# Kernel optimization log

Hardware: AMD Instinct MI355X
Metric: run time of the kernel (lower is better)

The kernel has to match this reference:

```python
import jax, jax.numpy as jnp
import numpy as np

N, T, H, NENV, L = 8192, 48, 256, 10, 2
NIN = 1 + 2 + NENV + 1 + 2  # x, coords(2), env(NENV), areas, bird_uv(2) = 16


def setup_inputs() -> dict:
    key = jax.random.key(0)
    ks = jax.random.split(key, 10)
    x = jax.random.normal(ks[0], (N, T), dtype=jnp.float32)
    coords = jax.random.normal(ks[1], (N, 2), dtype=jnp.float32)
    env = jax.random.normal(ks[2], (N, NENV, T), dtype=jnp.float32)
    areas = jax.random.uniform(ks[3], (N,), dtype=jnp.float32)
    bird_uv = jax.random.normal(ks[4], (N, 2, T), dtype=jnp.float32)
    # input2hidden: Linear(NIN, H, bias=False), kaiming-normal (fan_in = NIN)
    W_in = jax.random.normal(ks[5], (H, NIN), dtype=jnp.float32) * np.sqrt(2.0 / NIN)
    # LSTMCell params per layer: weight_ih [4H,H], weight_hh [4H,H], biases [4H]
    k_lstm = 1.0 / np.sqrt(H)
    W_ih = jax.random.uniform(ks[6], (L, 4 * H, H), minval=-k_lstm, maxval=k_lstm, dtype=jnp.float32)
    W_hh = jax.random.uniform(ks[7], (L, 4 * H, H), minval=-k_lstm, maxval=k_lstm, dtype=jnp.float32)
    b_ih = jax.random.uniform(ks[8], (L, 4 * H), minval=-k_lstm, maxval=k_lstm, dtype=jnp.float32)
    b_hh = jax.random.uniform(ks[9], (L, 4 * H), minval=-k_lstm, maxval=k_lstm, dtype=jnp.float32)
    return {"x": x, "coords": coords, "env": env, "areas": areas, "bird_uv": bird_uv,
            "W_in": W_in, "W_ih": W_ih, "W_hh": W_hh, "b_ih": b_ih, "b_hh": b_hh}


def _lstm_cell(inp, h, c, w_ih, w_hh, bi, bh):
    # torch.nn.LSTMCell gate order: i, f, g, o
    gates = inp @ w_ih.T + bi + h @ w_hh.T + bh  # [N, 4H]
    i, f, g, o = jnp.split(gates, 4, axis=-1)
    i = jax.nn.sigmoid(i)
    f = jax.nn.sigmoid(f)
    g = jnp.tanh(g)
    o = jax.nn.sigmoid(o)
    c_new = f * c + i * g
    h_new = o * jnp.tanh(c_new)
    return h_new, c_new


def reference(x, coords, env, areas, bird_uv, W_in, W_ih, W_hh, b_ih, b_hh):
    # Build [N, NIN, T] feature tensor matching torch.cat([x, coords, env, areas, bird_uv], dim=1)
    feats = jnp.concatenate([
        x[:, None, :],                                            # [N,1,T]
        jnp.broadcast_to(coords[:, :, None], (N, 2, T)),          # [N,2,T]
        env,                                                      # [N,NENV,T]
        jnp.broadcast_to(areas[:, None, None], (N, 1, T)),        # [N,1,T]
        bird_uv,                                                  # [N,2,T]
    ], axis=1)
    # input2hidden applied to all timesteps at once: [T, N, H]
    proj = jnp.einsum('hf,nft->tnh', W_in, feats)

    def step(carry, inp_t):
        h, c = carry  # each [L, N, H]
        inp = inp_t
        hs, cs = [], []
        for l in range(L):  # dropout_p = 0 -> no dropout between layers
            hl, cl = _lstm_cell(inp, h[l], c[l], W_ih[l], W_hh[l], b_ih[l], b_hh[l])
            hs.append(hl)
            cs.append(cl)
            inp = hl
        return (jnp.stack(hs), jnp.stack(cs)), None

    h0 = jnp.zeros((L, N, H), dtype=x.dtype)
    c0 = jnp.zeros((L, N, H), dtype=x.dtype)
    (h, c), _ = jax.lax.scan(step, (h0, c0), proj)
    return h, c
```

## Files before the change

kernel.cpp:

```cpp
#include <hip/hip_runtime.h>
#include <hip/hip_bf16.h>
#include <cstdint>

#define NB 8192
#define TSTEPS 48

typedef __hip_bfloat16 bf16;
typedef short bf16x8 __attribute__((ext_vector_type(8)));
typedef float f32x4 __attribute__((ext_vector_type(4)));

__device__ __forceinline__ float sigf(float x) { return 1.0f / (1.0f + __expf(-x)); }
__device__ __forceinline__ float tanhf_fast(float x) { return 2.0f / (1.0f + __expf(-2.0f * x)) - 1.0f; }

__device__ __forceinline__ void gld_lds16(const void* g, void* l) {
  typedef const __attribute__((address_space(1))) unsigned int* gp_t;
  typedef __attribute__((address_space(3))) unsigned int* lp_t;
  __builtin_amdgcn_global_load_lds(reinterpret_cast<gp_t>(reinterpret_cast<uintptr_t>(g)),
                                   reinterpret_cast<lp_t>(reinterpret_cast<uintptr_t>(l)),
                                   16, 0, 0);
}

__global__ void feats_kernel(const float* __restrict__ x, const float* __restrict__ coords,
                             const float* __restrict__ env, const float* __restrict__ areas,
                             const float* __restrict__ bird, bf16* __restrict__ feats) {
  int idx = blockIdx.x * 256 + threadIdx.x;
  int n = idx & (NB - 1);
  int t = idx >> 13;
  __align__(16) bf16 v[32];
  v[0] = __float2bfloat16(x[n * TSTEPS + t]);
  v[1] = __float2bfloat16(coords[n * 2 + 0]);
  v[2] = __float2bfloat16(coords[n * 2 + 1]);
#pragma unroll
  for (int e = 0; e < 10; ++e) v[3 + e] = __float2bfloat16(env[(n * 10 + e) * TSTEPS + t]);
  v[13] = __float2bfloat16(areas[n]);
  v[14] = __float2bfloat16(bird[(n * 2 + 0) * TSTEPS + t]);
  v[15] = __float2bfloat16(bird[(n * 2 + 1) * TSTEPS + t]);
#pragma unroll
  for (int f = 16; f < 32; ++f) v[f] = __float2bfloat16(0.0f);
  bf16* dst = feats + (size_t)idx * 32;
#pragma unroll
  for (int c = 0; c < 4; ++c) ((bf16x8*)dst)[c] = ((const bf16x8*)v)[c];
}

__device__ __forceinline__ int orig_row(int jp) {
  int q = jp >> 7, g = (jp >> 5) & 3, s = jp & 31;
  return g * 256 + q * 32 + s;
}

__global__ void packA_kernel(const float* __restrict__ W_hh0, const float* __restrict__ W_ih0,
                             const float* __restrict__ W_in, bf16* __restrict__ WA) {
  int idx = blockIdx.x * 256 + threadIdx.x;
  int jp = idx / 288, col = idx % 288;
  int j = orig_row(jp);
  float val = 0.0f;
  if (col < 256) {
    val = W_hh0[j * 256 + col];
  } else if (col < 272) {
    int f = col - 256;
    float s = 0.0f;
    for (int k = 0; k < 256; ++k) s += W_ih0[j * 256 + k] * W_in[k * 16 + f];
    val = s;
  }
  WA[(size_t)jp * 288 + col] = __float2bfloat16(val);
}

__global__ void packB_kernel(const float* __restrict__ W_ih1, const float* __restrict__ W_hh1,
                             bf16* __restrict__ WB) {
  int idx = blockIdx.x * 256 + threadIdx.x;
  int jp = idx >> 9, col = idx & 511;
  int j = orig_row(jp);
  float val = (col < 256) ? W_ih1[j * 256 + col] : W_hh1[j * 256 + (col - 256)];
  WB[(size_t)jp * 512 + col] = __float2bfloat16(val);
}

__global__ void packBias_kernel(const float* __restrict__ b_ih, const float* __restrict__ b_hh,
                                float* __restrict__ bA, float* __restrict__ bB) {
  int idx = blockIdx.x * 256 + threadIdx.x;
  int layer = idx >> 10, jp = idx & 1023;
  int j = orig_row(jp);
  float v = b_ih[layer * 1024 + j] + b_hh[layer * 1024 + j];
  if (layer == 0) bA[jp] = v; else bB[jp] = v;
}

__global__ __launch_bounds__(256, 4) void lstm_step(
    const bf16* __restrict__ h0r, bf16* __restrict__ h0w,
    const bf16* __restrict__ h1r, bf16* __restrict__ h1w,
    const bf16* __restrict__ feats,
    const bf16* __restrict__ WA, const bf16* __restrict__ WB,
    const float* __restrict__ bA, const float* __restrict__ bB,
    float* __restrict__ c0, float* __restrict__ c1,
    float* __restrict__ out, int tA, int tB, int phase0, int lastA, int lastB) {
  __shared__ float Gs[64 * 132];
  bf16* As = (bf16*)Gs;
  bf16* Bs = As + 128 * 32;

  const int tid = threadIdx.x;
  const int wid = tid >> 6, lane = tid & 63;
  const int quad = lane >> 4, l16 = lane & 15;
  const int mb = (wid >> 1) * 64, nb = (wid & 1) * 64;
  const int rowbase = blockIdx.x * 128;
  const int q = blockIdx.y;
  const int isA = blockIdx.z + phase0;

  const bf16* Wp = isA ? WA : WB;
  const int KW = isA ? 288 : 512;
  const int KITERS = isA ? 9 : 16;
  const int t = isA ? tA : tB;

  f32x4 acc[4][4];
#pragma unroll
  for (int i = 0; i < 4; ++i)
#pragma unroll
    for (int j = 0; j < 4; ++j) acc[i][j] = f32x4{0.f, 0.f, 0.f, 0.f};

  const int arow = wid * 32 + (lane >> 2);
  const int achunk = (lane & 3) * 8;
  const bf16* WGrow = Wp + (size_t)(q * 128 + arow) * KW + achunk;
  bf16* lA = As + wid * 1024;
  bf16* lB = Bs + wid * 1024;

  for (int kb = 0; kb < KITERS; ++kb) {
    const bf16* Arow;
    int astr;
    if (isA && kb == 8) {
      Arow = feats + ((size_t)t * NB + rowbase) * 32;
      astr = 32;
    } else {
      const bf16* src = (!isA && kb >= 8) ? (h1r + (kb - 8) * 32) : (h0r + kb * 32);
      Arow = src + (size_t)rowbase * 256;
      astr = 256;
    }
    const bf16* ga = Arow + (size_t)arow * astr + achunk;
    const bf16* gb = WGrow + kb * 32;
    gld_lds16(ga, lA);
    gld_lds16(ga + (size_t)16 * astr, lA + 512);
    gld_lds16(gb, lB);
    gld_lds16(gb + (size_t)16 * KW, lB + 512);
    __syncthreads();
    bf16x8 af[4], bfr[4];
#pragma unroll
    for (int i = 0; i < 4; ++i) af[i] = *(const bf16x8*)&As[(mb + i * 16 + l16) * 32 + quad * 8];
#pragma unroll
    for (int j = 0; j < 4; ++j) bfr[j] = *(const bf16x8*)&Bs[(nb + j * 16 + l16) * 32 + quad * 8];
#pragma unroll
    for (int i = 0; i < 4; ++i)
#pragma unroll
      for (int j = 0; j < 4; ++j)
        acc[i][j] = __builtin_amdgcn_mfma_f32_16x16x32_bf16(af[i], bfr[j], acc[i][j], 0, 0, 0);
    __syncthreads();
  }

  const float* bias = isA ? bA : bB;
  float* cst = isA ? c0 : c1;
  bf16* hout = isA ? h0w : h1w;
  const int last = isA ? lastA : lastB;
  float* out_h = out + (size_t)(isA ? 0 : 1) * NB * 256;
  float* out_c = out + (size_t)(isA ? 2 : 3) * NB * 256;

  const int s = tid & 31;
  const int rg = tid >> 5;
  const float bi = bias[q * 128 + 0 + s];
  const float bf_ = bias[q * 128 + 32 + s];
  const float bg = bias[q * 128 + 64 + s];
  const float bo = bias[q * 128 + 96 + s];
  const int u = q * 32 + s;

  for (int half = 0; half < 2; ++half) {
    if ((wid >> 1) == half) {
#pragma unroll
      for (int i = 0; i < 4; ++i)
#pragma unroll
        for (int j = 0; j < 4; ++j)
#pragma unroll
          for (int r = 0; r < 4; ++r)
            Gs[(i * 16 + quad * 4 + r) * 132 + nb + j * 16 + l16] = acc[i][j][r];
    }
    __syncthreads();
#pragma unroll
    for (int it = 0; it < 8; ++it) {
      int rl = rg * 8 + it;
      int n = rowbase + half * 64 + rl;
      float gi = sigf(Gs[rl * 132 + 0 + s] + bi);
      float gf = sigf(Gs[rl * 132 + 32 + s] + bf_);
      float gg = tanhf_fast(Gs[rl * 132 + 64 + s] + bg);
      float go = sigf(Gs[rl * 132 + 96 + s] + bo);
      size_t ci = (size_t)n * 256 + u;
      float c = cst[ci];
      float cn = gf * c + gi * gg;
      float hn = go * tanhf_fast(cn);
      cst[ci] = cn;
      hout[ci] = __float2bfloat16(hn);
      if (last) {
        out_h[ci] = hn;
        out_c[ci] = cn;
      }
    }
    __syncthreads();
  }
}

extern "C" void kernel_launch(void* const* d_in, const int* in_sizes, int n_in,
                              void* d_out, int out_size, void* d_ws, size_t ws_size,
                              hipStream_t stream) {
  const float* x = (const float*)d_in[0];
  const float* coords = (const float*)d_in[1];
  const float* env = (const float*)d_in[2];
  const float* areas = (const float*)d_in[3];
  const float* bird = (const float*)d_in[4];
  const float* W_in = (const float*)d_in[5];
  const float* W_ih = (const float*)d_in[6];
  const float* W_hh = (const float*)d_in[7];
  const float* b_ih = (const float*)d_in[8];
  const float* b_hh = (const float*)d_in[9];
  float* out = (float*)d_out;

  const size_t MB = 1 << 20;
  char* w0 = (char*)d_ws;
  auto H0 = [&](int i) { return (bf16*)(w0 + (size_t)i * 8 * MB); };
  auto H1 = [&](int i) { return (bf16*)(w0 + 4 * MB + (size_t)i * 8 * MB); };
  float* c0 = (float*)(w0 + 16 * MB);
  float* c1 = (float*)(w0 + 24 * MB);
  bf16* feats = (bf16*)(w0 + 32 * MB);
  bf16* WA = (bf16*)(w0 + 56 * MB);
  bf16* WB = (bf16*)(w0 + 57 * MB);
  float* bA = (float*)(w0 + 58 * MB);
  float* bB = (float*)(w0 + 58 * MB + 4096);

  hipMemsetAsync(w0 + 8 * MB, 0, 24 * MB, stream);

  feats_kernel<<<(NB * TSTEPS) / 256, 256, 0, stream>>>(x, coords, env, areas, bird, feats);
  packA_kernel<<<(1024 * 288) / 256, 256, 0, stream>>>(W_hh, W_ih, W_in, WA);
  packB_kernel<<<(1024 * 512) / 256, 256, 0, stream>>>(W_ih + 1024 * 256, W_hh + 1024 * 256, WB);
  packBias_kernel<<<2048 / 256, 256, 0, stream>>>(b_ih, b_hh, bA, bB);

  lstm_step<<<dim3(64, 8, 1), 256, 0, stream>>>(
      H0(1), H0(0), H1(0), H1(1), feats, WA, WB, bA, bB, c0, c1, out,
      0, 0, 1, 0, 0);
  for (int s2 = 0; s2 <= 46; ++s2) {
    int pa = (s2 + 1) & 1, pb = s2 & 1;
    lstm_step<<<dim3(64, 8, 2), 256, 0, stream>>>(
        H0(pb), H0(pa), H1(pa), H1(pb), feats, WA, WB, bA, bB, c0, c1, out,
        s2 + 1, s2, 0, (s2 == 46), 0);
  }
  lstm_step<<<dim3(64, 8, 1), 256, 0, stream>>>(
      H0(1), H0(0), H1(0), H1(1), feats, WA, WB, bA, bB, c0, c1, out,
      0, 47, 0, 0, 1);
}
```

Baseline: 1.492 ms.

## Replace per-timestep launches with persistent LSTM kernel using per-row-group atomic barriers

Swaps the chain of 49 per-step kernel launches for a single persistent kernel of 512 blocks. Each block loops over all timesteps and synchronises with the other 8 blocks of its row group through global atomic counters and spin-waits. Cell states now stay in registers instead of round-tripping through global memory, which removes launch gaps and c-state traffic. In exchange the layer-0 and layer-1 phases run serially within each block rather than wavefront-pipelined. It also relies on all 512 blocks being co-resident, or it deadlocks until the spin guard breaks.

```diff
diff --git a/kernel.cpp b/kernel.cpp
--- a/kernel.cpp
+++ b/kernel.cpp
@@ -18,6 +18,14 @@
   __builtin_amdgcn_global_load_lds(reinterpret_cast<gp_t>(reinterpret_cast<uintptr_t>(g)),
                                    reinterpret_cast<lp_t>(reinterpret_cast<uintptr_t>(l)),
                                    16, 0, 0);
+}
+
+__device__ __forceinline__ void spin_ge(unsigned* p, unsigned target) {
+  int guard = 0;
+  while (__hip_atomic_load(p, __ATOMIC_RELAXED, __HIP_MEMORY_SCOPE_AGENT) < target) {
+    __builtin_amdgcn_s_sleep(2);
+    if (++guard > 20000000) break;
+  }
 }
 
 __global__ void feats_kernel(const float* __restrict__ x, const float* __restrict__ coords,
@@ -82,14 +90,13 @@
   if (layer == 0) bA[jp] = v; else bB[jp] = v;
 }
 
-__global__ __launch_bounds__(256, 4) void lstm_step(
-    const bf16* __restrict__ h0r, bf16* __restrict__ h0w,
-    const bf16* __restrict__ h1r, bf16* __restrict__ h1w,
+__global__ __launch_bounds__(256, 2) void lstm_persistent(
+    bf16* __restrict__ h0, bf16* __restrict__ h1,
     const bf16* __restrict__ feats,
     const bf16* __restrict__ WA, const bf16* __restrict__ WB,
     const float* __restrict__ bA, const float* __restrict__ bB,
-    float* __restrict__ c0, float* __restrict__ c1,
-    float* __restrict__ out, int tA, int tB, int phase0, int lastA, int lastB) {
+    unsigned* __restrict__ cntA, unsigned* __restrict__ cntB,
+    float* __restrict__ out) {
   __shared__ float Gs[64 * 132];
   bf16* As = (bf16*)Gs;
   bf16* Bs = As + 128 * 32;
@@ -98,104 +105,185 @@
   const int wid = tid >> 6, lane = tid & 63;
   const int quad = lane >> 4, l16 = lane & 15;
   const int mb = (wid >> 1) * 64, nb = (wid & 1) * 64;
-  const int rowbase = blockIdx.x * 128;
-  const int q = blockIdx.y;
-  const int isA = blockIdx.z + phase0;
-
-  const bf16* Wp = isA ? WA : WB;
-  const int KW = isA ? 288 : 512;
-  const int KITERS = isA ? 9 : 16;
-  const int t = isA ? tA : tB;
-
-  f32x4 acc[4][4];
-#pragma unroll
-  for (int i = 0; i < 4; ++i)
-#pragma unroll
-    for (int j = 0; j < 4; ++j) acc[i][j] = f32x4{0.f, 0.f, 0.f, 0.f};
+  const int rg = blockIdx.x >> 3;
+  const int q = blockIdx.x & 7;
+  const int rowbase = rg * 128;
 
   const int arow = wid * 32 + (lane >> 2);
   const int achunk = (lane & 3) * 8;
-  const bf16* WGrow = Wp + (size_t)(q * 128 + arow) * KW + achunk;
   bf16* lA = As + wid * 1024;
   bf16* lB = Bs + wid * 1024;
-
-  for (int kb = 0; kb < KITERS; ++kb) {
-    const bf16* Arow;
-    int astr;
-    if (isA && kb == 8) {
-      Arow = feats + ((size_t)t * NB + rowbase) * 32;
-      astr = 32;
-    } else {
-      const bf16* src = (!isA && kb >= 8) ? (h1r + (kb - 8) * 32) : (h0r + kb * 32);
-      Arow = src + (size_t)rowbase * 256;
-      astr = 256;
-    }
-    const bf16* ga = Arow + (size_t)arow * astr + achunk;
-    const bf16* gb = WGrow + kb * 32;
-    gld_lds16(ga, lA);
-    gld_lds16(ga + (size_t)16 * astr, lA + 512);
-    gld_lds16(gb, lB);
-    gld_lds16(gb + (size_t)16 * KW, lB + 512);
+  const bf16* WArow = WA + (size_t)(q * 128 + arow) * 288 + achunk;
+  const bf16* WBrow = WB + (size_t)(q * 128 + arow) * 512 + achunk;
+
+  const int s = tid & 31;
+  const int rg8 = tid >> 5;
+  const float biA = bA[q * 128 + s], bfA = bA[q * 128 + 32 + s];
+  const float bgA = bA[q * 128 + 64 + s], boA = bA[q * 128 + 96 + s];
+  const float biB = bB[q * 128 + s], bfB = bB[q * 128 + 32 + s];
+  const float bgB = bB[q * 128 + 64 + s], boB = bB[q * 128 + 96 + s];
+  const int u = q * 32 + s;
+  const size_t NH = (size_t)NB * 256;
+
+  float c0r[16], c1r[16];
+#pragma unroll
+  for (int i = 0; i < 16; ++i) { c0r[i] = 0.f; c1r[i] = 0.f; }
+
+  f32x4 acc[4][4];
+
+#pragma unroll 1
+  for (int t = 0; t < TSTEPS; ++t) {
+    const int slotW = t & 1, slotR = slotW ^ 1;
+    const bf16* h0r_ = h0 + (size_t)slotR * NH;
+    bf16* h0w_ = h0 + (size_t)slotW * NH;
+    const bf16* h1r_ = h1 + (size_t)slotR * NH;
+    bf16* h1w_ = h1 + (size_t)slotW * NH;
+    const int last = (t == TSTEPS - 1);
+
+    if (tid == 0) {
+      if (t > 0) spin_ge(&cntA[rg], 8u * t);
+      __threadfence();
+    }
     __syncthreads();
-    bf16x8 af[4], bfr[4];
-#pragma unroll
-    for (int i = 0; i < 4; ++i) af[i] = *(const bf16x8*)&As[(mb + i * 16 + l16) * 32 + quad * 8];
-#pragma unroll
-    for (int j = 0; j < 4; ++j) bfr[j] = *(const bf16x8*)&Bs[(nb + j * 16 + l16) * 32 + quad * 8];
+
 #pragma unroll
     for (int i = 0; i < 4; ++i)
 #pragma unroll
-      for (int j = 0; j < 4; ++j)
-        acc[i][j] = __builtin_amdgcn_mfma_f32_16x16x32_bf16(af[i], bfr[j], acc[i][j], 0, 0, 0);
+      for (int j = 0; j < 4; ++j) acc[i][j] = f32x4{0.f, 0.f, 0.f, 0.f};
+
+    for (int kb = 0; kb < 9; ++kb) {
+      const bf16* ga;
+      int astr;
+      if (kb == 8) {
+        ga = feats + ((size_t)t * NB + rowbase + arow) * 32 + achunk;
+        astr = 32;
+      } else {
+        ga = h0r_ + (size_t)(rowbase + arow) * 256 + kb * 32 + achunk;
+        astr = 256;
+      }
+      const bf16* gb = WArow + kb * 32;
+      gld_lds16(ga, lA);
+      gld_lds16(ga + (size_t)16 * astr, lA + 512);
+      gld_lds16(gb, lB);
+      gld_lds16(gb + (size_t)16 * 288, lB + 512);
+      __syncthreads();
+      bf16x8 af[4], bfr[4];
+#pragma unroll
+      for (int i = 0; i < 4; ++i) af[i] = *(const bf16x8*)&As[(mb + i * 16 + l16) * 32 + quad * 8];
+#pragma unroll
+      for (int j = 0; j < 4; ++j) bfr[j] = *(const bf16x8*)&Bs[(nb + j * 16 + l16) * 32 + quad * 8];
+#pragma unroll
+      for (int i = 0; i < 4; ++i)
+#pragma unroll
+        for (int j = 0; j < 4; ++j)
+          acc[i][j] = __builtin_amdgcn_mfma_f32_16x16x32_bf16(af[i], bfr[j], acc[i][j], 0, 0, 0);
+      __syncthreads();
+    }
+
+    for (int half = 0; half < 2; ++half) {
+      if ((wid >> 1) == half) {
+#pragma unroll
+        for (int i = 0; i < 4; ++i)
+#pragma unroll
+          for (int j = 0; j < 4; ++j)
+#pragma unroll
+            for (int r = 0; r < 4; ++r)
+              Gs[(i * 16 + quad * 4 + r) * 132 + nb + j * 16 + l16] = acc[i][j][r];
+      }
+      __syncthreads();
+#pragma unroll
+      for (int it = 0; it < 8; ++it) {
+        int rl = rg8 * 8 + it;
+        int n = rowbase + half * 64 + rl;
+        float gi = sigf(Gs[rl * 132 + 0 + s] + biA);
+        float gf = sigf(Gs[rl * 132 + 32 + s] + bfA);
+        float gg = tanhf_fast(Gs[rl * 132 + 64 + s] + bgA);
+        float go = sigf(Gs[rl * 132 + 96 + s] + boA);
+        float cn = gf * c0r[half * 8 + it] + gi * gg;
+        float hn = go * tanhf_fast(cn);
+        c0r[half * 8 + it] = cn;
+        size_t ci = (size_t)n * 256 + u;
+        h0w_[ci] = __float2bfloat16(hn);
+        if (last) {
+          out[ci] = hn;
+          out[2 * NH + ci] = cn;
+        }
+      }
+      __syncthreads();
+    }
+
+    if (tid == 0) {
+      __threadfence();
+      __hip_atomic_fetch_add(&cntA[rg], 1u, __ATOMIC_RELEASE, __HIP_MEMORY_SCOPE_AGENT);
+      spin_ge(&cntA[rg], 8u * (t + 1));
+      if (t > 0) spin_ge(&cntB[rg], 8u * t);
+      __threadfence();
+    }
     __syncthreads();
-  }
-
-  const float* bias = isA ? bA : bB;
-  float* cst = isA ? c0 : c1;
-  bf16* hout = isA ? h0w : h1w;
-  const int last = isA ? lastA : lastB;
-  float* out_h = out + (size_t)(isA ? 0 : 1) * NB * 256;
-  float* out_c = out + (size_t)(isA ? 2 : 3) * NB * 256;
-
-  const int s = tid & 31;
-  const int rg = tid >> 5;
-  const float bi = bias[q * 128 + 0 + s];
-  const float bf_ = bias[q * 128 + 32 + s];
-  const float bg = bias[q * 128 + 64 + s];
-  const float bo = bias[q * 128 + 96 + s];
-  const int u = q * 32 + s;
-
-  for (int half = 0; half < 2; ++half) {
-    if ((wid >> 1) == half) {
+
+#pragma unroll
+    for (int i = 0; i < 4; ++i)
+#pragma unroll
+      for (int j = 0; j < 4; ++j) acc[i][j] = f32x4{0.f, 0.f, 0.f, 0.f};
+
+    for (int kb = 0; kb < 16; ++kb) {
+      const bf16* src = (kb >= 8) ? (h1r_ + (kb - 8) * 32) : (h0w_ + kb * 32);
+      const bf16* ga = src + (size_t)(rowbase + arow) * 256 + achunk;
+      const bf16* gb = WBrow + kb * 32;
+      gld_lds16(ga, lA);
+      gld_lds16(ga + (size_t)16 * 256, lA + 512);
+      gld_lds16(gb, lB);
+      gld_lds16(gb + (size_t)16 * 512, lB + 512);
+      __syncthreads();
+      bf16x8 af[4], bfr[4];
+#pragma unroll
+      for (int i = 0; i < 4; ++i) af[i] = *(const bf16x8*)&As[(mb + i * 16 + l16) * 32 + quad * 8];
+#pragma unroll
+      for (int j = 0; j < 4; ++j) bfr[j] = *(const bf16x8*)&Bs[(nb + j * 16 + l16) * 32 + quad * 8];
 #pragma unroll
       for (int i = 0; i < 4; ++i)
 #pragma unroll
         for (int j = 0; j < 4; ++j)
-#pragma unroll
-          for (int r = 0; r < 4; ++r)
-            Gs[(i * 16 + quad * 4 + r) * 132 + nb + j * 16 + l16] = acc[i][j][r];
-    }
-    __syncthreads();
-#pragma unroll
-    for (int it = 0; it < 8; ++it) {
-      int rl = rg * 8 + it;
-      int n = rowbase + half * 64 + rl;
-      float gi = sigf(Gs[rl * 132 + 0 + s] + bi);
-      float gf = sigf(Gs[rl * 132 + 32 + s] + bf_);
-      float gg = tanhf_fast(Gs[rl * 132 + 64 + s] + bg);
-      float go = sigf(Gs[rl * 132 + 96 + s] + bo);
-      size_t ci = (size_t)n * 256 + u;
-      float c = cst[ci];
-      float cn = gf * c + gi * gg;
-      float hn = go * tanhf_fast(cn);
-      cst[ci] = cn;
-      hout[ci] = __float2bfloat16(hn);
-      if (last) {
-        out_h[ci] = hn;
-        out_c[ci] = cn;
-      }
-    }
-    __syncthreads();
+          acc[i][j] = __builtin_amdgcn_mfma_f32_16x16x32_bf16(af[i], bfr[j], acc[i][j], 0, 0, 0);
+      __syncthreads();
+    }
+
+    for (int half = 0; half < 2; ++half) {
+      if ((wid >> 1) == half) {
+#pragma unroll
+        for (int i = 0; i < 4; ++i)
+#pragma unroll
+          for (int j = 0; j < 4; ++j)
+#pragma unroll
+            for (int r = 0; r < 4; ++r)
+              Gs[(i * 16 + quad * 4 + r) * 132 + nb + j * 16 + l16] = acc[i][j][r];
+      }
+      __syncthreads();
+#pragma unroll
+      for (int it = 0; it < 8; ++it) {
+        int rl = rg8 * 8 + it;
+        int n = rowbase + half * 64 + rl;
+        float gi = sigf(Gs[rl * 132 + 0 + s] + biB);
+        float gf = sigf(Gs[rl * 132 + 32 + s] + bfB);
+        float gg = tanhf_fast(Gs[rl * 132 + 64 + s] + bgB);
+        float go = sigf(Gs[rl * 132 + 96 + s] + boB);
+        float cn = gf * c1r[half * 8 + it] + gi * gg;
+        float hn = go * tanhf_fast(cn);
+        c1r[half * 8 + it] = cn;
+        size_t ci = (size_t)n * 256 + u;
+        h1w_[ci] = __float2bfloat16(hn);
+        if (last) {
+          out[NH + ci] = hn;
+          out[3 * NH + ci] = cn;
+        }
+      }
+      __syncthreads();
+    }
+
+    if (tid == 0) {
+      __threadfence();
+      __hip_atomic_fetch_add(&cntB[rg], 1u, __ATOMIC_RELEASE, __HIP_MEMORY_SCOPE_AGENT);
+    }
   }
 }
 
@@ -216,33 +304,22 @@
 
   const size_t MB = 1 << 20;
   char* w0 = (char*)d_ws;
-  auto H0 = [&](int i) { return (bf16*)(w0 + (size_t)i * 8 * MB); };
-  auto H1 = [&](int i) { return (bf16*)(w0 + 4 * MB + (size_t)i * 8 * MB); };
-  float* c0 = (float*)(w0 + 16 * MB);
-  float* c1 = (float*)(w0 + 24 * MB);
-  bf16* feats = (bf16*)(w0 + 32 * MB);
-  bf16* WA = (bf16*)(w0 + 56 * MB);
-  bf16* WB = (bf16*)(w0 + 57 * MB);
-  float* bA = (float*)(w0 + 58 * MB);
-  float* bB = (float*)(w0 + 58 * MB + 4096);
-
-  hipMemsetAsync(w0 + 8 * MB, 0, 24 * MB, stream);
+  bf16* h0 = (bf16*)w0;
+  bf16* h1 = (bf16*)(w0 + 8 * MB);
+  unsigned* cntA = (unsigned*)(w0 + 16 * MB);
+  unsigned* cntB = cntA + 64;
+  bf16* feats = (bf16*)(w0 + 17 * MB);
+  bf16* WA = (bf16*)(w0 + 41 * MB);
+  bf16* WB = (bf16*)(w0 + 42 * MB);
+  float* bA = (float*)(w0 + 43 * MB);
+  float* bB = (float*)(w0 + 43 * MB + 4096);
+
+  hipMemsetAsync(w0, 0, 16 * MB + 4096, stream);
 
   feats_kernel<<<(NB * TSTEPS) / 256, 256, 0, stream>>>(x, coords, env, areas, bird, feats);
   packA_kernel<<<(1024 * 288) / 256, 256, 0, stream>>>(W_hh, W_ih, W_in, WA);
   packB_kernel<<<(1024 * 512) / 256, 256, 0, stream>>>(W_ih + 1024 * 256, W_hh + 1024 * 256, WB);
   packBias_kernel<<<2048 / 256, 256, 0, stream>>>(b_ih, b_hh, bA, bB);
 
-  lstm_step<<<dim3(64, 8, 1), 256, 0, stream>>>(
-      H0(1), H0(0), H1(0), H1(1), feats, WA, WB, bA, bB, c0, c1, out,
-      0, 0, 1, 0, 0);
-  for (int s2 = 0; s2 <= 46; ++s2) {
-    int pa = (s2 + 1) & 1, pb = s2 & 1;
-    lstm_step<<<dim3(64, 8, 2), 256, 0, stream>>>(
-        H0(pb), H0(pa), H1(pa), H1(pb), feats, WA, WB, bA, bB, c0, c1, out,
-        s2 + 1, s2, 0, (s2 == 46), 0);
-  }
-  lstm_step<<<dim3(64, 8, 1), 256, 0, stream>>>(
-      H0(1), H0(0), H1(0), H1(1), feats, WA, WB, bA, bB, c0, c1, out,
-      0, 47, 0, 0, 1);
-}
+  lstm_persistent<<<512, 256, 0, stream>>>(h0, h1, feats, WA, WB, bA, bB, cntA, cntB, out);
+}
```

Measured after the change: 4.930 ms. 3.3x slower.
